# Kernel tuning notes

Measured on AMD Instinct MI355X. Metric: run time of the kernel, lower is better.

Reference implementation:

```python
import jax, jax.numpy as jnp
import numpy as np

N_NODES = 100000
N_EDGES = 1600000
D_IN = 64
H = 64


def setup_inputs() -> dict:
    key = jax.random.key(0)
    ks = jax.random.split(key, 8)
    inp = {
        "x": jax.random.normal(ks[0], (N_NODES, D_IN), dtype=jnp.float32),
        "edge_index": jax.random.randint(ks[1], (2, N_EDGES), 0, N_NODES, dtype=jnp.int64),
        # layer 1 (SAGEConv): lin_l (aggregated neighbors, with bias), lin_r (root, no bias)
        "Wl1": jax.random.normal(ks[2], (D_IN, H), dtype=jnp.float32) / np.sqrt(D_IN),
        "bl1": jnp.zeros((H,), dtype=jnp.float32),
        "Wr1": jax.random.normal(ks[3], (D_IN, H), dtype=jnp.float32) / np.sqrt(D_IN),
        # layer 2
        "Wl2": jax.random.normal(ks[4], (H, H), dtype=jnp.float32) / np.sqrt(H),
        "bl2": jnp.zeros((H,), dtype=jnp.float32),
        "Wr2": jax.random.normal(ks[5], (H, H), dtype=jnp.float32) / np.sqrt(H),
        "Wfc": jax.random.normal(ks[6], (H, 1), dtype=jnp.float32) / np.sqrt(H),
        "bfc": jnp.zeros((1,), dtype=jnp.float32),
    }
    return inp


def _sage_conv(h, src, dst, inv_deg, Wl, bl, Wr):
    # mean-aggregate neighbor features: scatter-add messages then normalize by in-degree
    agg = jax.ops.segment_sum(h[src], dst, num_segments=N_NODES)  # [N, d]
    agg = agg * inv_deg[:, None]
    return agg @ Wl + bl + h @ Wr


def reference(x, edge_index, Wl1, bl1, Wr1, Wl2, bl2, Wr2, Wfc, bfc):
    src, dst = edge_index[0], edge_index[1]
    deg = jax.ops.segment_sum(jnp.ones((src.shape[0],), dtype=x.dtype), dst,
                              num_segments=N_NODES)
    inv_deg = jnp.where(deg > 0, 1.0 / jnp.maximum(deg, 1.0), 0.0)

    h = jax.nn.relu(_sage_conv(x, src, dst, inv_deg, Wl1, bl1, Wr1))
    h = jax.nn.relu(_sage_conv(h, src, dst, inv_deg, Wl2, bl2, Wr2))
    return h @ Wfc + bfc  # [N, 1]
```

## Files before the change

kernel.cpp:

```cpp
#include <hip/hip_runtime.h>
#include <hip/hip_fp16.h>

#define NN 100000
#define NE 1600000
#define SHIFT 8
#define NBUCK 391
#define P1B   1024
#define EPB   1563

typedef _Float16 f16x8 __attribute__((ext_vector_type(8)));
typedef float f32x4 __attribute__((ext_vector_type(4)));
union H8U4 { f16x8 h; uint4 u; };

__device__ __forceinline__ int scan256(int* s, int t, int v) {
    s[t] = v;
    __syncthreads();
    for (int off = 1; off < 256; off <<= 1) {
        int add = (t >= off) ? s[t - off] : 0;
        __syncthreads();
        s[t] += add;
        __syncthreads();
    }
    return s[t];
}

__global__ __launch_bounds__(256) void k_hist(
    const float4* __restrict__ x4, ushort4* __restrict__ xh4,
    const float* __restrict__ Wl1, const float* __restrict__ Wr1, unsigned short* __restrict__ wt1,
    const float* __restrict__ Wl2, const float* __restrict__ Wr2, unsigned short* __restrict__ wt2,
    const int* __restrict__ dst, int* __restrict__ hist)
{
    __shared__ int h[NBUCK];
    int t = threadIdx.x, blk = blockIdx.x;

    const int n4 = NN * 16;
    const int per = (n4 + P1B - 1) / P1B;
    int cb = blk * per, ce = min(cb + per, n4);
    for (int i = cb + t; i < ce; i += 256) {
        float4 f = x4[i];
        _Float16 a = (_Float16)f.x, b = (_Float16)f.y, c = (_Float16)f.z, d = (_Float16)f.w;
        ushort4 u;
        u.x = *(unsigned short*)&a; u.y = *(unsigned short*)&b;
        u.z = *(unsigned short*)&c; u.w = *(unsigned short*)&d;
        xh4[i] = u;
    }
    if (blk < 64) {
        int idx = (blk & 31) * 256 + t;
        const float* Wl = (blk < 32) ? Wl1 : Wl2;
        const float* Wr = (blk < 32) ? Wr1 : Wr2;
        unsigned short* wt = (blk < 32) ? wt1 : wt2;
        int n = idx >> 7, k = idx & 127;
        float v = (k < 64) ? Wl[k * 64 + n] : Wr[(k - 64) * 64 + n];
        _Float16 hv = (_Float16)v;
        wt[idx] = *(unsigned short*)&hv;
    }

    for (int i = t; i < NBUCK; i += 256) h[i] = 0;
    __syncthreads();
    int eb = blk * EPB, ee = min(eb + EPB, NE);
    for (int e = eb + t; e < ee; e += 256) atomicAdd(&h[dst[e] >> SHIFT], 1);
    __syncthreads();
    for (int i = t; i < NBUCK; i += 256) hist[(size_t)blk * NBUCK + i] = h[i];
}

__global__ __launch_bounds__(256) void k_colscan(int* __restrict__ hist, int* __restrict__ total,
                                                 int* __restrict__ offsets) {
    __shared__ int sS[256];
    int b = blockIdx.x, t = threadIdx.x;
    int v0 = hist[(size_t)(t * 4 + 0) * NBUCK + b];
    int v1 = hist[(size_t)(t * 4 + 1) * NBUCK + b];
    int v2 = hist[(size_t)(t * 4 + 2) * NBUCK + b];
    int v3 = hist[(size_t)(t * 4 + 3) * NBUCK + b];
    int s = v0 + v1 + v2 + v3;
    int incl = scan256(sS, t, s);
    int ex = incl - s;
    hist[(size_t)(t * 4 + 0) * NBUCK + b] = ex;
    hist[(size_t)(t * 4 + 1) * NBUCK + b] = ex + v0;
    hist[(size_t)(t * 4 + 2) * NBUCK + b] = ex + v0 + v1;
    hist[(size_t)(t * 4 + 3) * NBUCK + b] = ex + v0 + v1 + v2;
    if (t == 255) total[b] = incl;
    if (b == 0 && t == 0) offsets[NN] = NE;
}

__global__ __launch_bounds__(256) void k_scatter(const int* __restrict__ src, const int* __restrict__ dst,
                                                 const int* __restrict__ hist, const int* __restrict__ total,
                                                 unsigned int* __restrict__ pairs) {
    __shared__ int cur[NBUCK];
    __shared__ int sS[256];
    int t = threadIdx.x, blk = blockIdx.x;
    int carry = 0;
#pragma unroll
    for (int c = 0; c < 2; c++) {
        int idx = c * 256 + t;
        int v = (idx < NBUCK) ? total[idx] : 0;
        int incl = scan256(sS, t, v);
        if (idx < NBUCK)
            cur[idx] = carry + incl - v + hist[(size_t)blk * NBUCK + idx];
        __syncthreads();
        carry += sS[255];
        __syncthreads();
    }
    int eb = blk * EPB, ee = min(eb + EPB, NE);
    for (int e = eb + t; e < ee; e += 256) {
        int d = dst[e];
        int pos = atomicAdd(&cur[d >> SHIFT], 1);
        pairs[pos] = (unsigned int)src[e] | ((unsigned int)(d & 255) << 17);
    }
}

__global__ __launch_bounds__(256) void k_bucket_csr(const unsigned int* __restrict__ pairs,
                                                    const int* __restrict__ total,
                                                    int* __restrict__ ssrc, int* __restrict__ offsets,
                                                    float* __restrict__ inv_deg) {
    __shared__ int cnt[256];
    __shared__ int sS[256];
    int b = blockIdx.x, t = threadIdx.x;
    int v = 0;
    for (int i = t; i < b; i += 256) v += total[i];
    sS[t] = v;
    __syncthreads();
    for (int s = 128; s > 0; s >>= 1) {
        if (t < s) sS[t] += sS[t + s];
        __syncthreads();
    }
    int beg = sS[0];
    int end = beg + total[b];
    __syncthreads();
    cnt[t] = 0;
    __syncthreads();
    for (int e = beg + t; e < end; e += 256) atomicAdd(&cnt[pairs[e] >> 17], 1);
    __syncthreads();
    int deg = cnt[t];
    int incl = scan256(sS, t, deg);
    int ex = incl - deg;
    int node = (b << SHIFT) + t;
    if (node < NN) {
        offsets[node] = beg + ex;
        inv_deg[node] = (deg > 0) ? (1.0f / (float)deg) : 0.0f;
    }
    __syncthreads();
    cnt[t] = beg + ex;
    __syncthreads();
    for (int e = beg + t; e < end; e += 256) {
        unsigned int pr = pairs[e];
        int pos = atomicAdd(&cnt[pr >> 17], 1);
        ssrc[pos] = (int)(pr & 0x1FFFFu);
    }
}

__device__ __forceinline__ void agg_pair(const uint4* __restrict__ featq, const int* __restrict__ ssrc,
                                         int beg0, int end0, int beg1, int end1,
                                         int c, int g, H8U4& acc0, H8U4& acc1) {
    int e0 = beg0, e1 = beg1;

    while (e0 + 16 <= end0 && e1 + 16 <= end1) {
        int i00 = ssrc[e0 + g], i01 = ssrc[e0 + 8 + g];
        int i10 = ssrc[e1 + g], i11 = ssrc[e1 + 8 + g];
        H8U4 q00, q01, q10, q11;
        q00.u = featq[(size_t)i00 * 8 + c];
        q01.u = featq[(size_t)i01 * 8 + c];
        q10.u = featq[(size_t)i10 * 8 + c];
        q11.u = featq[(size_t)i11 * 8 + c];
        acc0.h += q00.h; acc0.h += q01.h;
        acc1.h += q10.h; acc1.h += q11.h;
        e0 += 16; e1 += 16;
    }
    for (; e0 + 16 <= end0; e0 += 16) {
        int i0 = ssrc[e0 + g], i1 = ssrc[e0 + 8 + g];
        H8U4 q0, q1;
        q0.u = featq[(size_t)i0 * 8 + c];
        q1.u = featq[(size_t)i1 * 8 + c];
        acc0.h += q0.h; acc0.h += q1.h;
    }
    for (; e0 < end0; e0 += 8) {
        int m = end0 - e0;
        int idx = ssrc[e0 + (g < m ? g : m - 1)];
        H8U4 q;
        q.u = featq[(size_t)idx * 8 + c];
        if (g < m) acc0.h += q.h;
    }
    for (; e1 + 16 <= end1; e1 += 16) {
        int i0 = ssrc[e1 + g], i1 = ssrc[e1 + 8 + g];
        H8U4 q0, q1;
        q0.u = featq[(size_t)i0 * 8 + c];
        q1.u = featq[(size_t)i1 * 8 + c];
        acc1.h += q0.h; acc1.h += q1.h;
    }
    for (; e1 < end1; e1 += 8) {
        int m = end1 - e1;
        int idx = ssrc[e1 + (g < m ? g : m - 1)];
        H8U4 q;
        q.u = featq[(size_t)idx * 8 + c];
        if (g < m) acc1.h += q.h;
    }
}

template <bool FUSE_HEAD>
__global__ __launch_bounds__(256) void k_fused(const uint4* __restrict__ featq,
                                               const int* __restrict__ ssrc,
                                               const int* __restrict__ offsets, const float* __restrict__ inv_deg,
                                               const uint4* __restrict__ wtq,
                                               const float* __restrict__ bias,
                                               const float* __restrict__ Wfc, const float* __restrict__ bfc,
                                               float* __restrict__ out_f32, unsigned short* __restrict__ out_f16) {
    __shared__ uint4 sAgg[32][9];

    int tid = threadIdx.x;
    int wave = tid >> 6, lane = tid & 63;
    int base = blockIdx.x * 32;

    {
        int c = lane & 7, g = lane >> 3;
#pragma unroll 1
        for (int p = 0; p < 4; ++p) {
            int l0 = wave * 8 + p * 2;
            int node0 = base + l0;
            int node1 = node0 + 1;
            if (node0 >= NN) {
                if (g == 0) {
                    uint4 z = {0u, 0u, 0u, 0u};
                    sAgg[l0][c] = z;
                    sAgg[l0 + 1][c] = z;
                }
                continue;
            }
            bool has1 = node1 < NN;
            int beg0 = offsets[node0], end0 = offsets[node0 + 1];
            int beg1 = has1 ? offsets[node1] : 0, end1 = has1 ? offsets[node1 + 1] : 0;
            H8U4 acc0, acc1;
            acc0.h = (f16x8)(_Float16)0;
            acc1.h = (f16x8)(_Float16)0;
            agg_pair(featq, ssrc, beg0, end0, beg1, end1, c, g, acc0, acc1);

#pragma unroll
            for (int mask = 8; mask <= 32; mask <<= 1) {
                H8U4 o0, o1;
                o0.u.x = __shfl_xor(acc0.u.x, mask); o0.u.y = __shfl_xor(acc0.u.y, mask);
                o0.u.z = __shfl_xor(acc0.u.z, mask); o0.u.w = __shfl_xor(acc0.u.w, mask);
                o1.u.x = __shfl_xor(acc1.u.x, mask); o1.u.y = __shfl_xor(acc1.u.y, mask);
                o1.u.z = __shfl_xor(acc1.u.z, mask); o1.u.w = __shfl_xor(acc1.u.w, mask);
                acc0.h += o0.h;
                acc1.h += o1.h;
            }

            if (g == 0) {
                float s0 = inv_deg[node0];
                H8U4 r;
#pragma unroll
                for (int j = 0; j < 8; j++) r.h[j] = (_Float16)((float)acc0.h[j] * s0);
                sAgg[l0][c] = r.u;
                H8U4 r1;
                if (has1) {
                    float s1 = inv_deg[node1];
#pragma unroll
                    for (int j = 0; j < 8; j++) r1.h[j] = (_Float16)((float)acc1.h[j] * s1);
                } else {
                    r1.u = (uint4){0u, 0u, 0u, 0u};
                }
                sAgg[l0 + 1][c] = r1.u;
            }
        }
    }
    __syncthreads();

    if (wave >= 2) return;

    int nb = base + wave * 16;
    int m = lane & 15, quad = lane >> 4;
    int l = wave * 16 + m;

    int an = nb + m;
    if (an > NN - 1) an = NN - 1;
    H8U4 a[4];
    a[0].u = sAgg[l][quad];
    a[1].u = sAgg[l][4 + quad];
    a[2].u = featq[(size_t)an * 8 + quad];
    a[3].u = featq[(size_t)an * 8 + 4 + quad];

    f32x4 acc[4];
#pragma unroll
    for (int n = 0; n < 4; n++) acc[n] = (f32x4){0.f, 0.f, 0.f, 0.f};

#pragma unroll
    for (int ncol = 0; ncol < 4; ncol++) {
        int col = ncol * 16 + m;
#pragma unroll
        for (int ki = 0; ki < 4; ki++) {
            H8U4 b;
            b.u = wtq[col * 16 + ki * 4 + quad];
            acc[ncol] = __builtin_amdgcn_mfma_f32_16x16x32_f16(a[ki].h, b.h, acc[ncol], 0, 0, 0);
        }
    }

    float bs[4];
#pragma unroll
    for (int ncol = 0; ncol < 4; ncol++) bs[ncol] = bias[ncol * 16 + m];

    if (!FUSE_HEAD) {
#pragma unroll
        for (int r = 0; r < 4; r++) {
            int node = nb + quad * 4 + r;
            if (node < NN) {
#pragma unroll
                for (int ncol = 0; ncol < 4; ncol++) {
                    float v = fmaxf(acc[ncol][r] + bs[ncol], 0.f);
                    _Float16 hv = (_Float16)v;
                    out_f16[(size_t)node * 64 + ncol * 16 + m] = *(unsigned short*)&hv;
                }
            }
        }
    } else {
        float wf[4];
#pragma unroll
        for (int ncol = 0; ncol < 4; ncol++) wf[ncol] = Wfc[ncol * 16 + m];
#pragma unroll
        for (int r = 0; r < 4; r++) {
            int node = nb + quad * 4 + r;
            float partial = 0.f;
#pragma unroll
            for (int ncol = 0; ncol < 4; ncol++)
                partial += fmaxf(acc[ncol][r] + bs[ncol], 0.f) * wf[ncol];
            partial += __shfl_xor(partial, 1);
            partial += __shfl_xor(partial, 2);
            partial += __shfl_xor(partial, 4);
            partial += __shfl_xor(partial, 8);
            if (m == 0 && node < NN) out_f32[node] = partial + bfc[0];
        }
    }
}

extern "C" void kernel_launch(void* const* d_in, const int* in_sizes, int n_in,
                              void* d_out, int out_size, void* d_ws, size_t ws_size,
                              hipStream_t stream) {
    const float* x   = (const float*)d_in[0];
    const int*   ei  = (const int*)d_in[1];
    const float* Wl1 = (const float*)d_in[2];
    const float* bl1 = (const float*)d_in[3];
    const float* Wr1 = (const float*)d_in[4];
    const float* Wl2 = (const float*)d_in[5];
    const float* bl2 = (const float*)d_in[6];
    const float* Wr2 = (const float*)d_in[7];
    const float* Wfc = (const float*)d_in[8];
    const float* bfc = (const float*)d_in[9];
    float* out = (float*)d_out;

    const int* srcp = ei;
    const int* dstp = ei + NE;

    char* p = (char*)d_ws;
    auto carve = [&](size_t bytes) {
        char* q = p;
        p += (bytes + 255) & ~size_t(255);
        return q;
    };
    int*            offsets = (int*)carve((size_t)(NN + 1) * 4);
    float*          inv_deg = (float*)carve((size_t)NN * 4);
    int*            ssrc    = (int*)carve((size_t)NE * 4);
    unsigned short* xh      = (unsigned short*)carve((size_t)NN * 64 * 2);
    unsigned short* h1h     = (unsigned short*)carve((size_t)NN * 64 * 2);
    unsigned short* wt1     = (unsigned short*)carve(64 * 128 * 2);
    unsigned short* wt2     = (unsigned short*)carve(64 * 128 * 2);
    unsigned int*   pairs   = (unsigned int*)carve((size_t)NE * 4);
    int*            hist    = (int*)carve((size_t)P1B * NBUCK * 4);
    int*            total   = (int*)carve((size_t)NBUCK * 4);

    const int tile = (NN + 31) / 32;

    k_hist<<<P1B, 256, 0, stream>>>((const float4*)x, (ushort4*)xh,
                                    Wl1, Wr1, wt1, Wl2, Wr2, wt2, dstp, hist);
    k_colscan<<<NBUCK, 256, 0, stream>>>(hist, total, offsets);
    k_scatter<<<P1B, 256, 0, stream>>>(srcp, dstp, hist, total, pairs);
    k_bucket_csr<<<NBUCK, 256, 0, stream>>>(pairs, total, ssrc, offsets, inv_deg);

    k_fused<false><<<tile, 256, 0, stream>>>((const uint4*)xh, ssrc, offsets, inv_deg,
                                             (const uint4*)wt1, bl1, Wfc, bfc, nullptr, h1h);
    k_fused<true><<<tile, 256, 0, stream>>>((const uint4*)h1h, ssrc, offsets, inv_deg,
                                            (const uint4*)wt2, bl2, Wfc, bfc, out, nullptr);
}
```

Baseline: 245.0 us.

## Shrink buckets to 32 nodes and fuse CSR build into first SAGE layer

Bucket width drops from 256 to 32 nodes, so each bucket maps to exactly one 32-node tile of the fused layer kernel. The per-bucket CSR build (degree count, local scan, source scatter) now runs inside the layer-1 kernel, which removes the separate bucket_csr launch and lets that layer take offsets and degrees from registers. The histogram is stored as 16-bit counts to offset the growth to 3125 buckets, and colscan remaps block IDs across XCDs. In exchange, k_scatter now scans 3125 totals in every block, and the x conversion is split into its own launch.

Result: slower. 267.5 us (+9.2%).

```diff
diff --git a/kernel.cpp b/kernel.cpp
--- a/kernel.cpp
+++ b/kernel.cpp
@@ -3,8 +3,8 @@
 
 #define NN 100000
 #define NE 1600000
-#define SHIFT 8
-#define NBUCK 391
+#define SHIFT 5
+#define NBUCK 3125
 #define P1B   1024
 #define EPB   1563
 
@@ -24,15 +24,12 @@
     return s[t];
 }
 
-__global__ __launch_bounds__(256) void k_hist(
+__global__ __launch_bounds__(256) void k_convert(
     const float4* __restrict__ x4, ushort4* __restrict__ xh4,
     const float* __restrict__ Wl1, const float* __restrict__ Wr1, unsigned short* __restrict__ wt1,
-    const float* __restrict__ Wl2, const float* __restrict__ Wr2, unsigned short* __restrict__ wt2,
-    const int* __restrict__ dst, int* __restrict__ hist)
+    const float* __restrict__ Wl2, const float* __restrict__ Wr2, unsigned short* __restrict__ wt2)
 {
-    __shared__ int h[NBUCK];
     int t = threadIdx.x, blk = blockIdx.x;
-
     const int n4 = NN * 16;
     const int per = (n4 + P1B - 1) / P1B;
     int cb = blk * per, ce = min(cb + per, n4);
@@ -54,19 +51,27 @@
         _Float16 hv = (_Float16)v;
         wt[idx] = *(unsigned short*)&hv;
     }
-
+}
+
+__global__ __launch_bounds__(256) void k_hist(const int* __restrict__ dst, unsigned short* __restrict__ hist) {
+    __shared__ int h[NBUCK];
+    int t = threadIdx.x, blk = blockIdx.x;
     for (int i = t; i < NBUCK; i += 256) h[i] = 0;
     __syncthreads();
     int eb = blk * EPB, ee = min(eb + EPB, NE);
     for (int e = eb + t; e < ee; e += 256) atomicAdd(&h[dst[e] >> SHIFT], 1);
     __syncthreads();
-    for (int i = t; i < NBUCK; i += 256) hist[(size_t)blk * NBUCK + i] = h[i];
-}
-
-__global__ __launch_bounds__(256) void k_colscan(int* __restrict__ hist, int* __restrict__ total,
+    unsigned short* row = hist + (size_t)blk * NBUCK;
+    for (int i = t; i < NBUCK; i += 256) row[i] = (unsigned short)h[i];
+}
+
+__global__ __launch_bounds__(256) void k_colscan(unsigned short* __restrict__ hist, int* __restrict__ total,
                                                  int* __restrict__ offsets) {
     __shared__ int sS[256];
-    int b = blockIdx.x, t = threadIdx.x;
+    int bid = blockIdx.x, t = threadIdx.x;
+    const int q = NBUCK / 8, r = NBUCK % 8;
+    int xcd = bid & 7, i = bid >> 3;
+    int b = (xcd < r) ? xcd * (q + 1) + i : r * (q + 1) + (xcd - r) * q + i;
     int v0 = hist[(size_t)(t * 4 + 0) * NBUCK + b];
     int v1 = hist[(size_t)(t * 4 + 1) * NBUCK + b];
     int v2 = hist[(size_t)(t * 4 + 2) * NBUCK + b];
@@ -74,77 +79,45 @@
     int s = v0 + v1 + v2 + v3;
     int incl = scan256(sS, t, s);
     int ex = incl - s;
-    hist[(size_t)(t * 4 + 0) * NBUCK + b] = ex;
-    hist[(size_t)(t * 4 + 1) * NBUCK + b] = ex + v0;
-    hist[(size_t)(t * 4 + 2) * NBUCK + b] = ex + v0 + v1;
-    hist[(size_t)(t * 4 + 3) * NBUCK + b] = ex + v0 + v1 + v2;
+    hist[(size_t)(t * 4 + 0) * NBUCK + b] = (unsigned short)ex;
+    hist[(size_t)(t * 4 + 1) * NBUCK + b] = (unsigned short)(ex + v0);
+    hist[(size_t)(t * 4 + 2) * NBUCK + b] = (unsigned short)(ex + v0 + v1);
+    hist[(size_t)(t * 4 + 3) * NBUCK + b] = (unsigned short)(ex + v0 + v1 + v2);
     if (t == 255) total[b] = incl;
-    if (b == 0 && t == 0) offsets[NN] = NE;
+    if (bid == 0 && t == 0) offsets[NN] = NE;
 }
 
 __global__ __launch_bounds__(256) void k_scatter(const int* __restrict__ src, const int* __restrict__ dst,
-                                                 const int* __restrict__ hist, const int* __restrict__ total,
+                                                 const unsigned short* __restrict__ hist,
+                                                 const int* __restrict__ total,
+                                                 int* __restrict__ bucket_start,
                                                  unsigned int* __restrict__ pairs) {
     __shared__ int cur[NBUCK];
     __shared__ int sS[256];
     int t = threadIdx.x, blk = blockIdx.x;
     int carry = 0;
 #pragma unroll
-    for (int c = 0; c < 2; c++) {
+    for (int c = 0; c < 13; c++) {
         int idx = c * 256 + t;
         int v = (idx < NBUCK) ? total[idx] : 0;
         int incl = scan256(sS, t, v);
-        if (idx < NBUCK)
-            cur[idx] = carry + incl - v + hist[(size_t)blk * NBUCK + idx];
+        if (idx < NBUCK) cur[idx] = carry + incl - v;
         __syncthreads();
         carry += sS[255];
         __syncthreads();
     }
+    if (blk == 0) {
+        for (int i = t; i < NBUCK; i += 256) bucket_start[i] = cur[i];
+        if (t == 0) bucket_start[NBUCK] = NE;
+    }
+    const unsigned short* row = hist + (size_t)blk * NBUCK;
+    for (int i = t; i < NBUCK; i += 256) cur[i] += (int)row[i];
+    __syncthreads();
     int eb = blk * EPB, ee = min(eb + EPB, NE);
     for (int e = eb + t; e < ee; e += 256) {
         int d = dst[e];
         int pos = atomicAdd(&cur[d >> SHIFT], 1);
-        pairs[pos] = (unsigned int)src[e] | ((unsigned int)(d & 255) << 17);
-    }
-}
-
-__global__ __launch_bounds__(256) void k_bucket_csr(const unsigned int* __restrict__ pairs,
-                                                    const int* __restrict__ total,
-                                                    int* __restrict__ ssrc, int* __restrict__ offsets,
-                                                    float* __restrict__ inv_deg) {
-    __shared__ int cnt[256];
-    __shared__ int sS[256];
-    int b = blockIdx.x, t = threadIdx.x;
-    int v = 0;
-    for (int i = t; i < b; i += 256) v += total[i];
-    sS[t] = v;
-    __syncthreads();
-    for (int s = 128; s > 0; s >>= 1) {
-        if (t < s) sS[t] += sS[t + s];
-        __syncthreads();
-    }
-    int beg = sS[0];
-    int end = beg + total[b];
-    __syncthreads();
-    cnt[t] = 0;
-    __syncthreads();
-    for (int e = beg + t; e < end; e += 256) atomicAdd(&cnt[pairs[e] >> 17], 1);
-    __syncthreads();
-    int deg = cnt[t];
-    int incl = scan256(sS, t, deg);
-    int ex = incl - deg;
-    int node = (b << SHIFT) + t;
-    if (node < NN) {
-        offsets[node] = beg + ex;
-        inv_deg[node] = (deg > 0) ? (1.0f / (float)deg) : 0.0f;
-    }
-    __syncthreads();
-    cnt[t] = beg + ex;
-    __syncthreads();
-    for (int e = beg + t; e < end; e += 256) {
-        unsigned int pr = pairs[e];
-        int pos = atomicAdd(&cnt[pr >> 17], 1);
-        ssrc[pos] = (int)(pr & 0x1FFFFu);
+        pairs[pos] = (unsigned int)src[e] | ((unsigned int)(d & 31) << 17);
     }
 }
 
@@ -195,19 +168,56 @@
     }
 }
 
-template <bool FUSE_HEAD>
+template <bool BUILD>
 __global__ __launch_bounds__(256) void k_fused(const uint4* __restrict__ featq,
-                                               const int* __restrict__ ssrc,
-                                               const int* __restrict__ offsets, const float* __restrict__ inv_deg,
+                                               const unsigned int* __restrict__ pairs,
+                                               const int* __restrict__ bucket_start,
+                                               int* __restrict__ ssrc,
+                                               int* __restrict__ offsets, float* __restrict__ inv_deg,
                                                const uint4* __restrict__ wtq,
                                                const float* __restrict__ bias,
                                                const float* __restrict__ Wfc, const float* __restrict__ bfc,
                                                float* __restrict__ out_f32, unsigned short* __restrict__ out_f16) {
     __shared__ uint4 sAgg[32][9];
+    __shared__ int cnt[32];
+    __shared__ int cur[32];
 
     int tid = threadIdx.x;
     int wave = tid >> 6, lane = tid & 63;
-    int base = blockIdx.x * 32;
+    int b = blockIdx.x;
+    int base = b * 32;
+
+    int degL = 0, exL = 0, inclL = 0, segbeg = 0;
+    if (BUILD) {
+        segbeg = bucket_start[b];
+        int segend = bucket_start[b + 1];
+        if (tid < 32) cnt[tid] = 0;
+        __syncthreads();
+        for (int e = segbeg + tid; e < segend; e += 256) atomicAdd(&cnt[pairs[e] >> 17], 1);
+        __syncthreads();
+        int l5 = lane & 31;
+        degL = cnt[l5];
+        inclL = degL;
+#pragma unroll
+        for (int s = 1; s <= 16; s <<= 1) {
+            int v = __shfl_up(inclL, s);
+            if (l5 >= s) inclL += v;
+        }
+        exL = inclL - degL;
+        if (tid < 32) {
+            int node = base + tid;
+            offsets[node] = segbeg + exL;
+            inv_deg[node] = (degL > 0) ? (1.0f / (float)degL) : 0.0f;
+            cur[tid] = segbeg + exL;
+        }
+        __syncthreads();
+        for (int e = segbeg + tid; e < segend; e += 256) {
+            unsigned int pr = pairs[e];
+            int pos = atomicAdd(&cur[pr >> 17], 1);
+            ssrc[pos] = (int)(pr & 0x1FFFFu);
+        }
+        __syncthreads();
+    }
 
     {
         int c = lane & 7, g = lane >> 3;
@@ -225,8 +235,20 @@
                 continue;
             }
             bool has1 = node1 < NN;
-            int beg0 = offsets[node0], end0 = offsets[node0 + 1];
-            int beg1 = has1 ? offsets[node1] : 0, end1 = has1 ? offsets[node1 + 1] : 0;
+            int beg0, end0, beg1, end1;
+            float inv0, inv1;
+            if (BUILD) {
+                beg0 = segbeg + __shfl(exL, l0);   end0 = segbeg + __shfl(inclL, l0);
+                beg1 = segbeg + __shfl(exL, l0 + 1); end1 = segbeg + __shfl(inclL, l0 + 1);
+                int d0 = __shfl(degL, l0), d1 = __shfl(degL, l0 + 1);
+                inv0 = (d0 > 0) ? (1.0f / (float)d0) : 0.0f;
+                inv1 = (d1 > 0) ? (1.0f / (float)d1) : 0.0f;
+            } else {
+                beg0 = offsets[node0]; end0 = offsets[node0 + 1];
+                beg1 = has1 ? offsets[node1] : 0; end1 = has1 ? offsets[node1 + 1] : 0;
+                inv0 = inv_deg[node0];
+                inv1 = has1 ? inv_deg[node1] : 0.0f;
+            }
             H8U4 acc0, acc1;
             acc0.h = (f16x8)(_Float16)0;
             acc1.h = (f16x8)(_Float16)0;
@@ -244,16 +266,14 @@
             }
 
             if (g == 0) {
-                float s0 = inv_deg[node0];
                 H8U4 r;
 #pragma unroll
-                for (int j = 0; j < 8; j++) r.h[j] = (_Float16)((float)acc0.h[j] * s0);
+                for (int j = 0; j < 8; j++) r.h[j] = (_Float16)((float)acc0.h[j] * inv0);
                 sAgg[l0][c] = r.u;
                 H8U4 r1;
                 if (has1) {
-                    float s1 = inv_deg[node1];
-#pragma unroll
-                    for (int j = 0; j < 8; j++) r1.h[j] = (_Float16)((float)acc1.h[j] * s1);
+#pragma unroll
+                    for (int j = 0; j < 8; j++) r1.h[j] = (_Float16)((float)acc1.h[j] * inv1);
                 } else {
                     r1.u = (uint4){0u, 0u, 0u, 0u};
                 }
@@ -286,9 +306,9 @@
         int col = ncol * 16 + m;
 #pragma unroll
         for (int ki = 0; ki < 4; ki++) {
-            H8U4 b;
-            b.u = wtq[col * 16 + ki * 4 + quad];
-            acc[ncol] = __builtin_amdgcn_mfma_f32_16x16x32_f16(a[ki].h, b.h, acc[ncol], 0, 0, 0);
+            H8U4 bb;
+            bb.u = wtq[col * 16 + ki * 4 + quad];
+            acc[ncol] = __builtin_amdgcn_mfma_f32_16x16x32_f16(a[ki].h, bb.h, acc[ncol], 0, 0, 0);
         }
     }
 
@@ -296,7 +316,7 @@
 #pragma unroll
     for (int ncol = 0; ncol < 4; ncol++) bs[ncol] = bias[ncol * 16 + m];
 
-    if (!FUSE_HEAD) {
+    if (BUILD) {
 #pragma unroll
         for (int r = 0; r < 4; r++) {
             int node = nb + quad * 4 + r;
@@ -361,19 +381,20 @@
     unsigned short* wt1     = (unsigned short*)carve(64 * 128 * 2);
     unsigned short* wt2     = (unsigned short*)carve(64 * 128 * 2);
     unsigned int*   pairs   = (unsigned int*)carve((size_t)NE * 4);
-    int*            hist    = (int*)carve((size_t)P1B * NBUCK * 4);
+    unsigned short* hist    = (unsigned short*)carve((size_t)P1B * NBUCK * 2);
     int*            total   = (int*)carve((size_t)NBUCK * 4);
-
-    const int tile = (NN + 31) / 32;
-
-    k_hist<<<P1B, 256, 0, stream>>>((const float4*)x, (ushort4*)xh,
-                                    Wl1, Wr1, wt1, Wl2, Wr2, wt2, dstp, hist);
+    int*            bucket_start = (int*)carve((size_t)(NBUCK + 1) * 4);
+
+    k_convert<<<P1B, 256, 0, stream>>>((const float4*)x, (ushort4*)xh,
+                                       Wl1, Wr1, wt1, Wl2, Wr2, wt2);
+    k_hist<<<P1B, 256, 0, stream>>>(dstp, hist);
     k_colscan<<<NBUCK, 256, 0, stream>>>(hist, total, offsets);
-    k_scatter<<<P1B, 256, 0, stream>>>(srcp, dstp, hist, total, pairs);
-    k_bucket_csr<<<NBUCK, 256, 0, stream>>>(pairs, total, ssrc, offsets, inv_deg);
-
-    k_fused<false><<<tile, 256, 0, stream>>>((const uint4*)xh, ssrc, offsets, inv_deg,
-                                             (const uint4*)wt1, bl1, Wfc, bfc, nullptr, h1h);
-    k_fused<true><<<tile, 256, 0, stream>>>((const uint4*)h1h, ssrc, offsets, inv_deg,
-                                            (const uint4*)wt2, bl2, Wfc, bfc, out, nullptr);
-}
+    k_scatter<<<P1B, 256, 0, stream>>>(srcp, dstp, hist, total, bucket_start, pairs);
+
+    k_fused<true><<<NBUCK, 256, 0, stream>>>((const uint4*)xh, pairs, bucket_start, ssrc,
+                                             offsets, inv_deg, (const uint4*)wt1, bl1,
+                                             Wfc, bfc, nullptr, h1h);
+    k_fused<false><<<NBUCK, 256, 0, stream>>>((const uint4*)h1h, pairs, bucket_start, ssrc,
+                                              offsets, inv_deg, (const uint4*)wt2, bl2,
+                                              Wfc, bfc, out, nullptr);
+}
```
